# Kernel optimization log

Hardware: AMD Instinct MI355X
Metric: run time of the kernel (lower is better)

## Reference

```python
import jax, jax.numpy as jnp
import numpy as np

HID = 512
NUM_NODES = 100000
N_BATCH = 20000


def _gru_cell(x, h, W_ih, W_hh, b_ih, b_hh):
    # torch nn.GRU single-step cell; gate order r, z, n
    gi = x @ W_ih.T + b_ih            # [N, 3H]
    gh = h @ W_hh.T + b_hh            # [N, 3H]
    i_r, i_z, i_n = jnp.split(gi, 3, axis=-1)
    h_r, h_z, h_n = jnp.split(gh, 3, axis=-1)
    r = jax.nn.sigmoid(i_r + h_r)
    z = jax.nn.sigmoid(i_z + h_z)
    n = jnp.tanh(i_n + r * h_n)
    return (1.0 - z) * n + z * h


def setup_inputs() -> dict:
    key = jax.random.key(0)
    ks = jax.random.split(key, 12)
    s = 1.0 / np.sqrt(HID)
    inp = {
        'conv_emb': jax.random.normal(ks[0], (N_BATCH, HID), jnp.float32),
        'static_table': jax.random.normal(ks[1], (NUM_NODES, HID), jnp.float32),
        'dynamic_table': jax.random.normal(ks[2], (NUM_NODES, 2, HID), jnp.float32),
        'W_ih0': jax.random.normal(ks[3], (3 * HID, 2 * HID), jnp.float32) * s,
        'W_hh0': jax.random.normal(ks[4], (3 * HID, HID), jnp.float32) * s,
        'b_ih0': jax.random.normal(ks[5], (3 * HID,), jnp.float32) * s,
        'b_hh0': jax.random.normal(ks[6], (3 * HID,), jnp.float32) * s,
        'W_ih1': jax.random.normal(ks[7], (3 * HID, HID), jnp.float32) * s,
        'W_hh1': jax.random.normal(ks[8], (3 * HID, HID), jnp.float32) * s,
        'b_ih1': jax.random.normal(ks[9], (3 * HID,), jnp.float32) * s,
        'b_hh1': jax.random.normal(ks[10], (3 * HID,), jnp.float32) * s,
        'nids': jnp.arange(N_BATCH, dtype=jnp.int32),  # unique global node ids
    }
    return inp


def reference(conv_emb, static_table, dynamic_table,
              W_ih0, W_hh0, b_ih0, b_hh0,
              W_ih1, W_hh1, b_ih1, b_hh1, nids):
    # gather: static embeddings for batch nodes, concat with conv output
    x = jnp.concatenate([conv_emb, static_table[nids]], axis=-1)  # [N, 2H]
    h0 = dynamic_table[nids]                                      # [N, L, H]
    # single-step 2-layer GRU (seq_len == 1)
    h_new0 = _gru_cell(x, h0[:, 0], W_ih0, W_hh0, b_ih0, b_hh0)   # [N, H]
    h_new1 = _gru_cell(h_new0, h0[:, 1], W_ih1, W_hh1, b_ih1, b_hh1)
    hn = jnp.stack([h_new0, h_new1], axis=1)                      # [N, L, H]
    # scatter updated hidden states back into the persistent table
    updated_table = dynamic_table.at[nids].set(hn)                # [num_nodes, L, H]
    return updated_table
```

## Files before the change

### kernel.cpp

```cpp
#include <hip/hip_runtime.h>

#define NB 20000
#define NNODES 100000
#define MB2 79
#define MP2 (MB2*256)
#define NBITW 3125
#define NGEMM (MB2*8)

typedef unsigned short u16;
typedef __bf16 bf16x8 __attribute__((ext_vector_type(8)));
typedef float f32x4 __attribute__((ext_vector_type(4)));

__device__ __forceinline__ u16 f2bf(float f) {
  union { float f; unsigned u; } v; v.f = f;
  unsigned r = v.u + 0x7fffu + ((v.u >> 16) & 1u);
  return (u16)(r >> 16);
}
__device__ __forceinline__ float bf2f(u16 b) {
  union { unsigned u; float f; } v; v.u = ((unsigned)b) << 16;
  return v.f;
}

__global__ void prep_bt0i(const float* __restrict__ Wih, const float* __restrict__ Whh,
                          u16* __restrict__ Bt) {
  int idx = blockIdx.x * 256 + threadIdx.x;
  if (idx >= 2048 * 384) return;
  int jg = idx / 384;
  int k = (idx % 384) * 4;
  int j = jg >> 2, g = jg & 3;
  float4 v = make_float4(0.f, 0.f, 0.f, 0.f);
  if (g < 2) {
    int row = g * 512 + j;
    v = (k < 1024) ? *(const float4*)(Wih + (size_t)row * 1024 + k)
                   : *(const float4*)(Whh + (size_t)row * 512 + (k - 1024));
  } else if (g == 2) {
    if (k < 1024) v = *(const float4*)(Wih + (size_t)(1024 + j) * 1024 + k);
  } else {
    if (k >= 1024) v = *(const float4*)(Whh + (size_t)(1024 + j) * 512 + (k - 1024));
  }
  ushort4 b; b.x = f2bf(v.x); b.y = f2bf(v.y); b.z = f2bf(v.z); b.w = f2bf(v.w);
  *(ushort4*)(Bt + (size_t)jg * 1536 + k) = b;
}

__global__ void prep_bt1i(const float* __restrict__ Wih, const float* __restrict__ Whh,
                          u16* __restrict__ Bt) {
  int idx = blockIdx.x * 256 + threadIdx.x;
  if (idx >= 2048 * 256) return;
  int jg = idx / 256;
  int k = (idx % 256) * 4;
  int j = jg >> 2, g = jg & 3;
  float4 v = make_float4(0.f, 0.f, 0.f, 0.f);
  if (g < 2) {
    int row = g * 512 + j;
    v = (k < 512) ? *(const float4*)(Wih + (size_t)row * 512 + k)
                  : *(const float4*)(Whh + (size_t)row * 512 + (k - 512));
  } else if (g == 2) {
    if (k < 512) v = *(const float4*)(Wih + (size_t)(1024 + j) * 512 + k);
  } else {
    if (k >= 512) v = *(const float4*)(Whh + (size_t)(1024 + j) * 512 + (k - 512));
  }
  ushort4 b; b.x = f2bf(v.x); b.y = f2bf(v.y); b.z = f2bf(v.z); b.w = f2bf(v.w);
  *(ushort4*)(Bt + (size_t)jg * 1024 + k) = b;
}

__global__ void prep_a(const float* __restrict__ conv, const float* __restrict__ stat,
                       const float* __restrict__ dyn, const int* __restrict__ nids,
                       u16* __restrict__ A0, u16* __restrict__ A1) {
  int idx = blockIdx.x * 256 + threadIdx.x;
  int n = idx >> 9;
  int c = (idx & 511) * 4;
  if (n >= MP2) return;
  float4 v = make_float4(0.f, 0.f, 0.f, 0.f);
  if (n < NB) {
    size_t nid = (size_t)nids[n];
    if (c < 512)        v = *(const float4*)(conv + (size_t)n * 512 + c);
    else if (c < 1024)  v = *(const float4*)(stat + nid * 512 + (c - 512));
    else if (c < 1536)  v = *(const float4*)(dyn + nid * 1024 + (c - 1024));
    else                v = *(const float4*)(dyn + nid * 1024 + 512 + (c - 1536));
  }
  ushort4 b; b.x = f2bf(v.x); b.y = f2bf(v.y); b.z = f2bf(v.z); b.w = f2bf(v.w);
  if (c < 1536) *(ushort4*)(A0 + (size_t)n * 1536 + c) = b;
  else          *(ushort4*)(A1 + (size_t)n * 1024 + (c - 1024)) = b;
  if (n >= NB && c < 512) *(ushort4*)(A1 + (size_t)n * 1024 + c) = b;
}

__global__ void zero_bits(unsigned* __restrict__ bits) {
  int i = blockIdx.x * 256 + threadIdx.x;
  if (i < NBITW) bits[i] = 0;
}
__global__ void set_bits(const int* __restrict__ nids, unsigned* __restrict__ bits) {
  int i = blockIdx.x * 256 + threadIdx.x;
  if (i < NB) {
    int nid = nids[i];
    atomicOr(&bits[nid >> 5], 1u << (nid & 31));
  }
}

template <int K, int LAYER>
__global__ __launch_bounds__(512, 2)
void gemmt(const u16* __restrict__ A, const u16* __restrict__ Bt,
           const float* __restrict__ bih, const float* __restrict__ bhh,
           const u16* __restrict__ hsrc, int hstride, const int* __restrict__ nids,
           u16* __restrict__ a1out, float* __restrict__ out) {
  constexpr int NT = K / 64;
  __shared__ u16 S[2][2][2][8192];

  int bid = blockIdx.x;
  int bn = bid & 7, bm = bid >> 3;

  int t = threadIdx.x;
  int lane = t & 63, w = t >> 6;
  int fr = lane & 15, fq = lane >> 4;
  int wm = w >> 2, wn = w & 3;

  const u16* Ap = A + (size_t)bm * 256 * K;
  const u16* Bp = Bt + (size_t)bn * 256 * K;

  int srow[2], skc[2];
#pragma unroll
  for (int l = 0; l < 2; ++l) {
    int c = l * 512 + t;
    int p = c >> 4, up = c & 15;
    int u = up ^ ((p & 7) << 1);
    srow[l] = (p << 1) | (u & 1);
    skc[l] = u >> 1;
  }
  auto stage = [&](int kt) {
    char* base = (char*)S + (size_t)(kt & 1) * 65536;
#pragma unroll
    for (int m = 0; m < 2; ++m)
#pragma unroll
      for (int h = 0; h < 2; ++h)
#pragma unroll
        for (int l = 0; l < 2; ++l) {
          const u16* g = (m ? Bp : Ap) + (size_t)(h * 128 + srow[l]) * K + kt * 64 + skc[l] * 8;
          __builtin_amdgcn_global_load_lds(
              (const __attribute__((address_space(1))) void*)g,
              (__attribute__((address_space(3))) void*)
              (base + m * 32768 + h * 16384 + (l * 512 + t) * 16), 16, 0, 0);
        }
  };

  int swz = (((fr >> 1) & 7) << 1);
  int ub = ((fq << 1) | (fr & 1)) ^ swz;
  int offA[4], offA2[4], offB[4];
#pragma unroll
  for (int mi = 0; mi < 4; ++mi) {
    offA[mi]  = wm * 16384 + (mi * 8 + (fr >> 1)) * 256 + ub * 16;
    offA2[mi] = wm * 16384 + ((mi + 4) * 8 + (fr >> 1)) * 256 + ub * 16;
  }
#pragma unroll
  for (int nf = 0; nf < 4; ++nf)
    offB[nf] = 32768 + (wn >> 1) * 16384 +
               ((wn & 1) * 32 + nf * 8 + (fr >> 1)) * 256 + ub * 16;

  f32x4 acc[8][4] = {};

  stage(0);
  __syncthreads();

  for (int kt = 0; kt < NT; ++kt) {
    const char* sb = (const char*)S + (size_t)(kt & 1) * 65536;

    bf16x8 a0[4], b0[4], a1v[4];
#pragma unroll
    for (int mi = 0; mi < 4; ++mi) a0[mi] = *(const bf16x8*)(sb + offA[mi]);
#pragma unroll
    for (int nf = 0; nf < 4; ++nf) b0[nf] = *(const bf16x8*)(sb + offB[nf]);

    if (kt + 1 < NT) stage(kt + 1);

    __builtin_amdgcn_s_setprio(1);
#pragma unroll
    for (int mi = 0; mi < 4; ++mi)
#pragma unroll
      for (int nf = 0; nf < 4; ++nf)
        acc[mi][nf] = __builtin_amdgcn_mfma_f32_16x16x32_bf16(a0[mi], b0[nf],
                                                              acc[mi][nf], 0, 0, 0);
#pragma unroll
    for (int mi = 0; mi < 4; ++mi) a1v[mi] = *(const bf16x8*)(sb + offA2[mi]);
#pragma unroll
    for (int mi = 0; mi < 4; ++mi)
#pragma unroll
      for (int nf = 0; nf < 4; ++nf)
        acc[mi + 4][nf] = __builtin_amdgcn_mfma_f32_16x16x32_bf16(a1v[mi], b0[nf],
                                                                  acc[mi + 4][nf], 0, 0, 0);
#pragma unroll
    for (int mi = 0; mi < 4; ++mi) a0[mi] = *(const bf16x8*)(sb + (offA[mi] ^ 128));
#pragma unroll
    for (int nf = 0; nf < 4; ++nf) b0[nf] = *(const bf16x8*)(sb + (offB[nf] ^ 128));
#pragma unroll
    for (int mi = 0; mi < 4; ++mi)
#pragma unroll
      for (int nf = 0; nf < 4; ++nf)
        acc[mi][nf] = __builtin_amdgcn_mfma_f32_16x16x32_bf16(a0[mi], b0[nf],
                                                              acc[mi][nf], 0, 0, 0);
#pragma unroll
    for (int mi = 0; mi < 4; ++mi) a1v[mi] = *(const bf16x8*)(sb + (offA2[mi] ^ 128));
#pragma unroll
    for (int mi = 0; mi < 4; ++mi)
#pragma unroll
      for (int nf = 0; nf < 4; ++nf)
        acc[mi + 4][nf] = __builtin_amdgcn_mfma_f32_16x16x32_bf16(a1v[mi], b0[nf],
                                                                  acc[mi + 4][nf], 0, 0, 0);
    __builtin_amdgcn_s_setprio(0);

    __syncthreads();
  }

  int gg = fr & 3, jj = fr >> 2;
  float bias[4];
#pragma unroll
  for (int nf = 0; nf < 4; ++nf) {
    int j = bn * 64 + wn * 16 + nf * 4 + jj;
    bias[nf] = (gg == 0) ? bih[j] + bhh[j]
             : (gg == 1) ? bih[512 + j] + bhh[512 + j]
             : (gg == 2) ? bih[1024 + j] : bhh[1024 + j];
  }
#pragma unroll
  for (int mi = 0; mi < 8; ++mi) {
    int row = bm * 256 + wm * 128 + mi * 16 + fq * 4 + gg;
#pragma unroll
    for (int nf = 0; nf < 4; ++nf) {
      float v[4], v1[4], v2[4];
#pragma unroll
      for (int r = 0; r < 4; ++r) v[r] = acc[mi][nf][r] + bias[nf];
#pragma unroll
      for (int i = 0; i < 4; ++i) {
        float o = __shfl_xor(v[i ^ 2], 2);
        v1[i] = ((i ^ gg) & 2) ? o : v[i];
      }
#pragma unroll
      for (int i = 0; i < 4; ++i) {
        float o = __shfl_xor(v1[i ^ 1], 1);
        v2[i] = ((i ^ gg) & 1) ? o : v1[i];
      }
      if (row < NB) {
        int j = bn * 64 + wn * 16 + nf * 4 + jj;
        float rr = 1.f / (1.f + __expf(-v2[0]));
        float zz = 1.f / (1.f + __expf(-v2[1]));
        float nn = tanhf(fmaf(rr, v2[3], v2[2]));
        float h = bf2f(hsrc[(size_t)row * hstride + j]);
        float hp = (1.f - zz) * nn + zz * h;
        if (LAYER == 0) a1out[(size_t)row * 1024 + j] = f2bf(hp);
        out[(size_t)nids[row] * 1024 + LAYER * 512 + j] = hp;
      }
    }
  }
}

__global__ void copy_skip(const float4* __restrict__ src, float4* __restrict__ dst,
                          const unsigned* __restrict__ bits) {
  const size_t total = (size_t)NNODES * 256;
  for (size_t i = (size_t)blockIdx.x * 256 + threadIdx.x; i < total;
       i += (size_t)gridDim.x * 256) {
    int row = (int)(i >> 8);
    if (!((bits[row >> 5] >> (row & 31)) & 1u)) {
      dst[i] = src[i];
    }
  }
}

extern "C" void kernel_launch(void* const* d_in, const int* in_sizes, int n_in,
                              void* d_out, int out_size, void* d_ws, size_t ws_size,
                              hipStream_t stream) {
  const float* conv = (const float*)d_in[0];
  const float* stat = (const float*)d_in[1];
  const float* dyn  = (const float*)d_in[2];
  const float* Wih0 = (const float*)d_in[3];
  const float* Whh0 = (const float*)d_in[4];
  const float* bih0 = (const float*)d_in[5];
  const float* bhh0 = (const float*)d_in[6];
  const float* Wih1 = (const float*)d_in[7];
  const float* Whh1 = (const float*)d_in[8];
  const float* bih1 = (const float*)d_in[9];
  const float* bhh1 = (const float*)d_in[10];
  const int*   nids = (const int*)d_in[11];
  float* out = (float*)d_out;

  char* ws = (char*)d_ws;
  u16* A0  = (u16*)ws;
  u16* A1  = (u16*)(ws + 62128128);
  u16* Bt0 = (u16*)(ws + 103546880);
  u16* Bt1 = (u16*)(ws + 109838336);
  unsigned* bits = (unsigned*)(ws + 114032640);

  zero_bits<<<(NBITW + 255) / 256, 256, 0, stream>>>(bits);
  set_bits<<<(NB + 255) / 256, 256, 0, stream>>>(nids, bits);
  prep_bt0i<<<3072, 256, 0, stream>>>(Wih0, Whh0, Bt0);
  prep_bt1i<<<2048, 256, 0, stream>>>(Wih1, Whh1, Bt1);
  prep_a<<<(MP2 * 512) / 256, 256, 0, stream>>>(conv, stat, dyn, nids, A0, A1);

  gemmt<1536, 0><<<NGEMM, 512, 0, stream>>>(A0, Bt0, bih0, bhh0,
                                            A0 + 1024, 1536, nids, A1, out);
  gemmt<1024, 1><<<NGEMM, 512, 0, stream>>>(A1, Bt1, bih1, bhh1,
                                            A1 + 512, 1024, nids, (u16*)nullptr, out);

  copy_skip<<<2048, 256, 0, stream>>>((const float4*)dyn, (float4*)out, bits);
}
```

Before: 498.0 us.

## Fuse the table copy of untouched rows into the GEMM main loops

Removes the separate copy_skip kernel. The bulk copy of rows not in nids, from dynamic_table to the output, is split across the two GEMM launches: the first 60000 rows go to layer 0 and the rest to layer 1. Each block loads its slice of float4s into registers during each k-iteration and stores them one iteration later, so the memory-bound copy overlaps the MFMA-bound GEMM. The cost is extra registers and global traffic inside the GEMM loop, which could reduce occupancy or slow the matrix pipeline.

```diff
diff --git a/kernel.cpp b/kernel.cpp
--- a/kernel.cpp
+++ b/kernel.cpp
@@ -101,7 +101,9 @@
 void gemmt(const u16* __restrict__ A, const u16* __restrict__ Bt,
            const float* __restrict__ bih, const float* __restrict__ bhh,
            const u16* __restrict__ hsrc, int hstride, const int* __restrict__ nids,
-           u16* __restrict__ a1out, float* __restrict__ out) {
+           u16* __restrict__ a1out, float* __restrict__ out,
+           const float4* __restrict__ src4, float4* __restrict__ dst4,
+           const unsigned* __restrict__ bits, int cbeg, int per, int cendTot) {
   constexpr int NT = K / 64;
   __shared__ u16 S[2][2][2][8192];
 
@@ -115,6 +117,9 @@
 
   const u16* Ap = A + (size_t)bm * 256 * K;
   const u16* Bp = Bt + (size_t)bn * 256 * K;
+
+  int cslice = cbeg + bid * per;
+  int cend2 = cslice + per; if (cend2 > cendTot) cend2 = cendTot;
 
   int srow[2], skc[2];
 #pragma unroll
@@ -156,6 +161,11 @@
 
   f32x4 acc[8][4] = {};
 
+  float4 creg0, creg1;
+  int cprev0 = 0, cprev1 = 0;
+  bool cv0 = false, cv1 = false;
+  unsigned cb0 = 0, cb1 = 0;
+
   stage(0);
   __syncthreads();
 
@@ -169,6 +179,16 @@
     for (int nf = 0; nf < 4; ++nf) b0[nf] = *(const bf16x8*)(sb + offB[nf]);
 
     if (kt + 1 < NT) stage(kt + 1);
+
+    if (cv0 && !((cb0 >> ((cprev0 >> 8) & 31)) & 1u)) dst4[cprev0] = creg0;
+    if (cv1 && !((cb1 >> ((cprev1 >> 8) & 31)) & 1u)) dst4[cprev1] = creg1;
+    {
+      int ci = cslice + (kt * 512 + t) * 2;
+      cv0 = ci < cend2; cv1 = ci + 1 < cend2;
+      cprev0 = ci; cprev1 = ci + 1;
+      if (cv0) { creg0 = src4[ci];     cb0 = bits[(ci >> 8) >> 5]; }
+      if (cv1) { creg1 = src4[ci + 1]; cb1 = bits[((ci + 1) >> 8) >> 5]; }
+    }
 
     __builtin_amdgcn_s_setprio(1);
 #pragma unroll
@@ -207,6 +227,9 @@
 
     __syncthreads();
   }
+
+  if (cv0 && !((cb0 >> ((cprev0 >> 8) & 31)) & 1u)) dst4[cprev0] = creg0;
+  if (cv1 && !((cb1 >> ((cprev1 >> 8) & 31)) & 1u)) dst4[cprev1] = creg1;
 
   int gg = fr & 3, jj = fr >> 2;
   float bias[4];
@@ -245,18 +268,6 @@
         if (LAYER == 0) a1out[(size_t)row * 1024 + j] = f2bf(hp);
         out[(size_t)nids[row] * 1024 + LAYER * 512 + j] = hp;
       }
-    }
-  }
-}
-
-__global__ void copy_skip(const float4* __restrict__ src, float4* __restrict__ dst,
-                          const unsigned* __restrict__ bits) {
-  const size_t total = (size_t)NNODES * 256;
-  for (size_t i = (size_t)blockIdx.x * 256 + threadIdx.x; i < total;
-       i += (size_t)gridDim.x * 256) {
-    int row = (int)(i >> 8);
-    if (!((bits[row >> 5] >> (row & 31)) & 1u)) {
-      dst[i] = src[i];
     }
   }
 }
@@ -291,10 +302,16 @@
   prep_bt1i<<<2048, 256, 0, stream>>>(Wih1, Whh1, Bt1);
   prep_a<<<(MP2 * 512) / 256, 256, 0, stream>>>(conv, stat, dyn, nids, A0, A1);
 
+  const int C0 = 60000 * 256, C1 = 100000 * 256;
+  const int per0 = (C0 + NGEMM - 1) / NGEMM;
+  const int per1 = ((C1 - C0) + NGEMM - 1) / NGEMM;
+
   gemmt<1536, 0><<<NGEMM, 512, 0, stream>>>(A0, Bt0, bih0, bhh0,
-                                            A0 + 1024, 1536, nids, A1, out);
+                                            A0 + 1024, 1536, nids, A1, out,
+                                            (const float4*)dyn, (float4*)out, bits,
+                                            0, per0, C0);
   gemmt<1024, 1><<<NGEMM, 512, 0, stream>>>(A1, Bt1, bih1, bhh1,
-                                            A1 + 512, 1024, nids, (u16*)nullptr, out);
-
-  copy_skip<<<2048, 256, 0, stream>>>((const float4*)dyn, (float4*)out, bits);
-}
+                                            A1 + 512, 1024, nids, (u16*)nullptr, out,
+                                            (const float4*)dyn, (float4*)out, bits,
+                                            C0, per1, C1);
+}
```

Result: slower. 546.6 us (+9.8%).

## Skip zero weight blocks in GRU GEMMs and split gate math into separate kernel

Applied to the files above, without the earlier changes.

The packed weight matrices are reordered so that each block column covers a single gate group. Each GEMM block now iterates only over the K range that holds nonzero weights, which avoids MFMA work on the zero-padded halves of the n-gate columns. The fused gate epilogue is replaced by writing bf16 pre-activations to a scratch buffer carved from the tail of the output. A separate elementwise gru_gates kernel then reads them back and applies the biases, sigmoid, tanh and the state update. The cost is an extra round trip through memory, uneven per-block work, and bf16 rounding of the pre-activations. The scratch buffer is also only safe when no batch node id maps into the output tail it occupies.

```diff
diff --git a/kernel.cpp b/kernel.cpp
--- a/kernel.cpp
+++ b/kernel.cpp
@@ -21,46 +21,44 @@
   return v.f;
 }
 
-__global__ void prep_bt0i(const float* __restrict__ Wih, const float* __restrict__ Whh,
+__global__ void prep_bt0d(const float* __restrict__ Wih, const float* __restrict__ Whh,
                           u16* __restrict__ Bt) {
   int idx = blockIdx.x * 256 + threadIdx.x;
   if (idx >= 2048 * 384) return;
-  int jg = idx / 384;
+  int jc = idx / 384;
   int k = (idx % 384) * 4;
-  int j = jg >> 2, g = jg & 3;
   float4 v = make_float4(0.f, 0.f, 0.f, 0.f);
-  if (g < 2) {
-    int row = g * 512 + j;
+  if (jc < 1024) {
+    int row = (jc & 1) * 512 + (jc >> 1);
     v = (k < 1024) ? *(const float4*)(Wih + (size_t)row * 1024 + k)
                    : *(const float4*)(Whh + (size_t)row * 512 + (k - 1024));
-  } else if (g == 2) {
-    if (k < 1024) v = *(const float4*)(Wih + (size_t)(1024 + j) * 1024 + k);
+  } else if (jc < 1536) {
+    if (k < 1024) v = *(const float4*)(Wih + (size_t)jc * 1024 + k);
   } else {
-    if (k >= 1024) v = *(const float4*)(Whh + (size_t)(1024 + j) * 512 + (k - 1024));
+    if (k >= 1024) v = *(const float4*)(Whh + (size_t)(jc - 512) * 512 + (k - 1024));
   }
   ushort4 b; b.x = f2bf(v.x); b.y = f2bf(v.y); b.z = f2bf(v.z); b.w = f2bf(v.w);
-  *(ushort4*)(Bt + (size_t)jg * 1536 + k) = b;
-}
-
-__global__ void prep_bt1i(const float* __restrict__ Wih, const float* __restrict__ Whh,
+  *(ushort4*)(Bt + (size_t)jc * 1536 + k) = b;
+}
+
+__global__ void prep_bt1d(const float* __restrict__ Wih, const float* __restrict__ Whh,
                           u16* __restrict__ Bt) {
   int idx = blockIdx.x * 256 + threadIdx.x;
   if (idx >= 2048 * 256) return;
-  int jg = idx / 256;
+  int jc = idx / 256;
   int k = (idx % 256) * 4;
-  int j = jg >> 2, g = jg & 3;
   float4 v = make_float4(0.f, 0.f, 0.f, 0.f);
-  if (g < 2) {
-    int row = g * 512 + j;
+  if (jc < 1024) {
+    int row = (jc & 1) * 512 + (jc >> 1);
     v = (k < 512) ? *(const float4*)(Wih + (size_t)row * 512 + k)
                   : *(const float4*)(Whh + (size_t)row * 512 + (k - 512));
-  } else if (g == 2) {
-    if (k < 512) v = *(const float4*)(Wih + (size_t)(1024 + j) * 512 + k);
+  } else if (jc < 1536) {
+    if (k < 512) v = *(const float4*)(Wih + (size_t)jc * 512 + k);
   } else {
-    if (k >= 512) v = *(const float4*)(Whh + (size_t)(1024 + j) * 512 + (k - 512));
+    if (k >= 512) v = *(const float4*)(Whh + (size_t)(jc - 512) * 512 + (k - 512));
   }
   ushort4 b; b.x = f2bf(v.x); b.y = f2bf(v.y); b.z = f2bf(v.z); b.w = f2bf(v.w);
-  *(ushort4*)(Bt + (size_t)jg * 1024 + k) = b;
+  *(ushort4*)(Bt + (size_t)jc * 1024 + k) = b;
 }
 
 __global__ void prep_a(const float* __restrict__ conv, const float* __restrict__ stat,
@@ -96,17 +94,17 @@
   }
 }
 
-template <int K, int LAYER>
+template <int K>
 __global__ __launch_bounds__(512, 2)
-void gemmt(const u16* __restrict__ A, const u16* __restrict__ Bt,
-           const float* __restrict__ bih, const float* __restrict__ bhh,
-           const u16* __restrict__ hsrc, int hstride, const int* __restrict__ nids,
-           u16* __restrict__ a1out, float* __restrict__ out) {
-  constexpr int NT = K / 64;
+void gemmd(const u16* __restrict__ A, const u16* __restrict__ Bt, u16* __restrict__ C) {
   __shared__ u16 S[2][2][2][8192];
 
   int bid = blockIdx.x;
-  int bn = bid & 7, bm = bid >> 3;
+  int bn = bid / MB2, bm = bid - bn * MB2;
+
+  int nt, k0;
+  if (K == 1536) { nt = bn < 4 ? 24 : (bn < 6 ? 16 : 8); k0 = bn < 6 ? 0 : 16; }
+  else           { nt = bn < 4 ? 16 : 8;                 k0 = bn >= 6 ? 8 : 0; }
 
   int t = threadIdx.x;
   int lane = t & 63, w = t >> 6;
@@ -156,10 +154,10 @@
 
   f32x4 acc[8][4] = {};
 
-  stage(0);
+  stage(k0);
   __syncthreads();
 
-  for (int kt = 0; kt < NT; ++kt) {
+  for (int kt = k0; kt < k0 + nt; ++kt) {
     const char* sb = (const char*)S + (size_t)(kt & 1) * 65536;
 
     bf16x8 a0[4], b0[4], a1v[4];
@@ -168,7 +166,7 @@
 #pragma unroll
     for (int nf = 0; nf < 4; ++nf) b0[nf] = *(const bf16x8*)(sb + offB[nf]);
 
-    if (kt + 1 < NT) stage(kt + 1);
+    if (kt + 1 < k0 + nt) stage(kt + 1);
 
     __builtin_amdgcn_s_setprio(1);
 #pragma unroll
@@ -209,14 +207,6 @@
   }
 
   int gg = fr & 3, jj = fr >> 2;
-  float bias[4];
-#pragma unroll
-  for (int nf = 0; nf < 4; ++nf) {
-    int j = bn * 64 + wn * 16 + nf * 4 + jj;
-    bias[nf] = (gg == 0) ? bih[j] + bhh[j]
-             : (gg == 1) ? bih[512 + j] + bhh[512 + j]
-             : (gg == 2) ? bih[1024 + j] : bhh[1024 + j];
-  }
 #pragma unroll
   for (int mi = 0; mi < 8; ++mi) {
     int row = bm * 256 + wm * 128 + mi * 16 + fq * 4 + gg;
@@ -224,7 +214,7 @@
     for (int nf = 0; nf < 4; ++nf) {
       float v[4], v1[4], v2[4];
 #pragma unroll
-      for (int r = 0; r < 4; ++r) v[r] = acc[mi][nf][r] + bias[nf];
+      for (int r = 0; r < 4; ++r) v[r] = acc[mi][nf][r];
 #pragma unroll
       for (int i = 0; i < 4; ++i) {
         float o = __shfl_xor(v[i ^ 2], 2);
@@ -235,17 +225,58 @@
         float o = __shfl_xor(v1[i ^ 1], 1);
         v2[i] = ((i ^ gg) & 1) ? o : v1[i];
       }
-      if (row < NB) {
-        int j = bn * 64 + wn * 16 + nf * 4 + jj;
-        float rr = 1.f / (1.f + __expf(-v2[0]));
-        float zz = 1.f / (1.f + __expf(-v2[1]));
-        float nn = tanhf(fmaf(rr, v2[3], v2[2]));
-        float h = bf2f(hsrc[(size_t)row * hstride + j]);
-        float hp = (1.f - zz) * nn + zz * h;
-        if (LAYER == 0) a1out[(size_t)row * 1024 + j] = f2bf(hp);
-        out[(size_t)nids[row] * 1024 + LAYER * 512 + j] = hp;
-      }
+      ushort4 cw; cw.x = f2bf(v2[0]); cw.y = f2bf(v2[1]);
+      cw.z = f2bf(v2[2]); cw.w = f2bf(v2[3]);
+      int colb = bn * 256 + wn * 64 + nf * 16 + jj * 4;
+      *(ushort4*)(C + (size_t)row * 2048 + colb) = cw;
     }
+  }
+}
+
+__global__ void gru_gates(const u16* __restrict__ C, const float* __restrict__ bih,
+                          const float* __restrict__ bhh, const u16* __restrict__ hsrc,
+                          int hstride, const int* __restrict__ nids, int layer,
+                          u16* __restrict__ a1out, float* __restrict__ out) {
+  int idx = blockIdx.x * 256 + threadIdx.x;
+  if (idx >= NB * 128) return;
+  int n = idx >> 7, jq = (idx & 127) << 2;
+  const u16* Cr = C + (size_t)n * 2048;
+  uint4 rzw = *(const uint4*)(Cr + 2 * jq);
+  ushort4 iv = *(const ushort4*)(Cr + 1024 + jq);
+  ushort4 hv = *(const ushort4*)(Cr + 1536 + jq);
+  ushort4 hh = *(const ushort4*)(hsrc + (size_t)n * hstride + jq);
+  float4 bri = *(const float4*)(bih + jq);
+  float4 brh = *(const float4*)(bhh + jq);
+  float4 bzi = *(const float4*)(bih + 512 + jq);
+  float4 bzh = *(const float4*)(bhh + 512 + jq);
+  float4 bni = *(const float4*)(bih + 1024 + jq);
+  float4 bnh = *(const float4*)(bhh + 1024 + jq);
+  unsigned wv[4] = {rzw.x, rzw.y, rzw.z, rzw.w};
+  float rg[4], zg[4];
+#pragma unroll
+  for (int k = 0; k < 4; ++k) {
+    rg[k] = bf2f((u16)(wv[k] & 0xffffu));
+    zg[k] = bf2f((u16)(wv[k] >> 16));
+  }
+  float ig[4] = {bf2f(iv.x), bf2f(iv.y), bf2f(iv.z), bf2f(iv.w)};
+  float hg[4] = {bf2f(hv.x), bf2f(hv.y), bf2f(hv.z), bf2f(hv.w)};
+  float h4[4] = {bf2f(hh.x), bf2f(hh.y), bf2f(hh.z), bf2f(hh.w)};
+  float fri[4] = {bri.x, bri.y, bri.z, bri.w}, frh[4] = {brh.x, brh.y, brh.z, brh.w};
+  float fzi[4] = {bzi.x, bzi.y, bzi.z, bzi.w}, fzh[4] = {bzh.x, bzh.y, bzh.z, bzh.w};
+  float fni[4] = {bni.x, bni.y, bni.z, bni.w}, fnh[4] = {bnh.x, bnh.y, bnh.z, bnh.w};
+  float o[4];
+#pragma unroll
+  for (int k = 0; k < 4; ++k) {
+    float r_ = 1.f / (1.f + __expf(-(rg[k] + fri[k] + frh[k])));
+    float z_ = 1.f / (1.f + __expf(-(zg[k] + fzi[k] + fzh[k])));
+    float nn = tanhf(fmaf(r_, hg[k] + fnh[k], ig[k] + fni[k]));
+    o[k] = fmaf(z_, h4[k] - nn, nn);
+  }
+  size_t nid = (size_t)nids[n];
+  *(float4*)(out + nid * 1024 + (size_t)layer * 512 + jq) = make_float4(o[0], o[1], o[2], o[3]);
+  if (a1out) {
+    ushort4 ob; ob.x = f2bf(o[0]); ob.y = f2bf(o[1]); ob.z = f2bf(o[2]); ob.w = f2bf(o[3]);
+    *(ushort4*)(a1out + (size_t)n * 1024 + jq) = ob;
   }
 }
 
@@ -285,16 +316,20 @@
   u16* Bt1 = (u16*)(ws + 109838336);
   unsigned* bits = (unsigned*)(ws + 114032640);
 
+  u16* Cb = (u16*)(out + (102400000 - 20709376));
+
   zero_bits<<<(NBITW + 255) / 256, 256, 0, stream>>>(bits);
   set_bits<<<(NB + 255) / 256, 256, 0, stream>>>(nids, bits);
-  prep_bt0i<<<3072, 256, 0, stream>>>(Wih0, Whh0, Bt0);
-  prep_bt1i<<<2048, 256, 0, stream>>>(Wih1, Whh1, Bt1);
+  prep_bt0d<<<3072, 256, 0, stream>>>(Wih0, Whh0, Bt0);
+  prep_bt1d<<<2048, 256, 0, stream>>>(Wih1, Whh1, Bt1);
   prep_a<<<(MP2 * 512) / 256, 256, 0, stream>>>(conv, stat, dyn, nids, A0, A1);
 
-  gemmt<1536, 0><<<NGEMM, 512, 0, stream>>>(A0, Bt0, bih0, bhh0,
-                                            A0 + 1024, 1536, nids, A1, out);
-  gemmt<1024, 1><<<NGEMM, 512, 0, stream>>>(A1, Bt1, bih1, bhh1,
-                                            A1 + 512, 1024, nids, (u16*)nullptr, out);
+  gemmd<1536><<<NGEMM, 512, 0, stream>>>(A0, Bt0, Cb);
+  gru_gates<<<(NB * 128) / 256, 256, 0, stream>>>(Cb, bih0, bhh0, A0 + 1024, 1536,
+                                                  nids, 0, A1, out);
+  gemmd<1024><<<NGEMM, 512, 0, stream>>>(A1, Bt1, Cb);
+  gru_gates<<<(NB * 128) / 256, 256, 0, stream>>>(Cb, bih1, bhh1, A1 + 512, 1024,
+                                                  nids, 1, (u16*)nullptr, out);
 
   copy_skip<<<2048, 256, 0, stream>>>((const float4*)dyn, (float4*)out, bits);
 }
```

Result: faster. 464.8 us (-6.7%).
